# Kernel tuning notes

Measured on AMD Instinct MI355X. Metric: run time of the kernel, lower is better.

## Reference

```python
import jax, jax.numpy as jnp
import numpy as np

HEAD_SIZE = 128
N_Q_HEADS = 32
N_KV_HEADS = 8
ROPE_THETA = 1000000.0
RMS_EPS = 1e-6


def rms_norm(x, w, eps=RMS_EPS):
    # normalize over last dim in fp32, like Qwen3RMSNorm
    xf = x.astype(jnp.float32)
    var = jnp.mean(xf * xf, axis=-1, keepdims=True)
    return w * (xf * jax.lax.rsqrt(var + eps)).astype(x.dtype)


def rope_cache(T, dim, theta=ROPE_THETA):
    half = dim // 2
    inv_freq = 1.0 / theta ** (jnp.arange(half, dtype=jnp.float32) / half)
    freqs = jnp.arange(T, dtype=jnp.float32)[:, None] * inv_freq[None, :]  # [T, half]
    emb = jnp.concatenate([freqs, freqs], axis=-1)  # [T, dim]
    return jnp.cos(emb), jnp.sin(emb)


def rotate_half(x):
    x1, x2 = jnp.split(x, 2, axis=-1)
    return jnp.concatenate([-x2, x1], axis=-1)


def setup_inputs() -> dict:
    key = jax.random.key(0)
    ks = jax.random.split(key, 5)
    B, T, C = 2, 2048, 4096
    s = 0.02
    return {
        "hidden_states": jax.random.normal(ks[0], (B, T, C), jnp.float32),
        "wq": jax.random.normal(ks[1], (N_Q_HEADS * HEAD_SIZE, C), jnp.float32) * s,
        "wk": jax.random.normal(ks[2], (N_KV_HEADS * HEAD_SIZE, C), jnp.float32) * s,
        "wv": jax.random.normal(ks[3], (N_KV_HEADS * HEAD_SIZE, C), jnp.float32) * s,
        "wo": jax.random.normal(ks[4], (C, N_Q_HEADS * HEAD_SIZE), jnp.float32) * s,
        "q_norm_w": jnp.ones((HEAD_SIZE,), jnp.float32),
        "k_norm_w": jnp.ones((HEAD_SIZE,), jnp.float32),
    }


def reference(hidden_states, wq, wk, wv, wo, q_norm_w, k_norm_w):
    B, T, C = hidden_states.shape
    D = HEAD_SIZE
    groups = N_Q_HEADS // N_KV_HEADS
    scale = D ** -0.5

    # projections -> [B, H, T, D]
    q = (hidden_states @ wq.T).reshape(B, T, N_Q_HEADS, D)
    k = (hidden_states @ wk.T).reshape(B, T, N_KV_HEADS, D)
    v = (hidden_states @ wv.T).reshape(B, T, N_KV_HEADS, D)

    q = rms_norm(q, q_norm_w).transpose(0, 2, 1, 3)
    k = rms_norm(k, k_norm_w).transpose(0, 2, 1, 3)
    v = v.transpose(0, 2, 1, 3)

    cos, sin = rope_cache(T, D)  # [T, D]
    cos = cos[None, None]  # broadcast over batch, heads
    sin = sin[None, None]
    q = q * cos + rotate_half(q) * sin
    k = k * cos + rotate_half(k) * sin

    # GQA repeat_kv: [B, Hkv, T, D] -> [B, Hq, T, D]
    k = jnp.repeat(k, groups, axis=1)
    v = jnp.repeat(v, groups, axis=1)

    # causal SDPA
    scores = jnp.einsum("bhqd,bhkd->bhqk", q, k) * scale
    causal = jnp.tril(jnp.ones((T, T), bool))
    scores = jnp.where(causal[None, None], scores, -jnp.inf)
    probs = jax.nn.softmax(scores, axis=-1)
    attn = jnp.einsum("bhqk,bhkd->bhqd", probs, v)

    attn = attn.transpose(0, 2, 1, 3).reshape(B, T, N_Q_HEADS * D)
    return attn @ wo.T
```

## Files before the change

### kernel.cpp

```cpp
#include <hip/hip_runtime.h>
#include <math.h>

typedef unsigned short u16;
typedef __attribute__((ext_vector_type(8))) short short8;
typedef __attribute__((ext_vector_type(4))) float f32x4;
typedef __attribute__((ext_vector_type(16))) float f32x16;

#define AS1 __attribute__((address_space(1)))
#define AS3 __attribute__((address_space(3)))

__device__ __forceinline__ void gload_lds16(const u16* g, u16* l) {
  __builtin_amdgcn_global_load_lds((AS1 void*)g, (AS3 void*)l, 16, 0, 0);
}

__device__ __forceinline__ float bf2f(u16 u) {
  union { unsigned i; float f; } c; c.i = ((unsigned)u) << 16; return c.f;
}
__device__ __forceinline__ u16 f2bf(float f) {
  union { float f; unsigned i; } c; c.f = f;
  unsigned r = c.i + 0x7fffu + ((c.i >> 16) & 1u);
  return (u16)(r >> 16);
}

__global__ __launch_bounds__(256)
void cvt_f32_bf16_k(const float* __restrict__ src, u16* __restrict__ dst, int n8)
{
  int i = blockIdx.x * blockDim.x + threadIdx.x;
  const int stride = gridDim.x * blockDim.x;
  for (; i < n8; i += stride) {
    float4 a = ((const float4*)src)[2 * i];
    float4 b = ((const float4*)src)[2 * i + 1];
    short8 o;
    o[0] = (short)f2bf(a.x); o[1] = (short)f2bf(a.y);
    o[2] = (short)f2bf(a.z); o[3] = (short)f2bf(a.w);
    o[4] = (short)f2bf(b.x); o[5] = (short)f2bf(b.y);
    o[6] = (short)f2bf(b.z); o[7] = (short)f2bf(b.w);
    ((short8*)dst)[i] = o;
  }
}

#define MFMA16(a, b, c) __builtin_amdgcn_mfma_f32_16x16x32_bf16((a), (b), (c), 0, 0, 0)

#define STAGE_H(panel, h, t, ldsb)                                          \
  { const u16* s_ = (panel) + (size_t)((h) * 128) * 4096 + (t) * 64;        \
    gload_lds16(s_,                   (ldsb) + ldst0);                      \
    gload_lds16(s_ + (size_t)64*4096, (ldsb) + 4096 + ldst0); }

#define PHASE(MB, STAGE_STMT, TAIL)                                         \
  {                                                                         \
    short8 a0k0 = *(const short8*)(aB + (MB)*1024 + aoff0);                 \
    short8 a0k1 = *(const short8*)(aB + (MB)*1024 + (aoff0 ^ 32));          \
    short8 a1k0 = *(const short8*)(aB + ((MB)+1)*1024 + aoff0);             \
    short8 a1k1 = *(const short8*)(aB + ((MB)+1)*1024 + (aoff0 ^ 32));      \
    STAGE_STMT                                                              \
    __builtin_amdgcn_s_barrier();                                           \
    asm volatile("s_waitcnt lgkmcnt(0)" ::: "memory");                      \
    __builtin_amdgcn_s_setprio(1);                                          \
    _Pragma("unroll")                                                       \
    for (int n = 0; n < 4; ++n) {                                           \
      acc[(MB)][n]   = MFMA16(a0k0, br[n][0], acc[(MB)][n]);                \
      acc[(MB)][n]   = MFMA16(a0k1, br[n][1], acc[(MB)][n]);                \
      acc[(MB)+1][n] = MFMA16(a1k0, br[n][0], acc[(MB)+1][n]);              \
      acc[(MB)+1][n] = MFMA16(a1k1, br[n][1], acc[(MB)+1][n]);              \
    }                                                                       \
    __builtin_amdgcn_s_setprio(0);                                          \
    TAIL                                                                    \
    __builtin_amdgcn_s_barrier();                                           \
  }

#define KTILE(BUF, T)                                                       \
  {                                                                         \
    const u16* aB = sA + (BUF) * 16384 + wr * 8192;                         \
    const u16* bB = sB + (BUF) * 16384 + (wc >> 1) * 8192;                  \
    u16* aO = sA + ((BUF) ^ 1) * 16384;                                     \
    u16* bO = sB + (BUF) * 16384;                                           \
    const bool st1 = (T) + 1 < NT, st2 = (T) + 2 < NT;                      \
    short8 br[4][2];                                                        \
    _Pragma("unroll")                                                       \
    for (int n = 0; n < 4; ++n) {                                           \
      br[n][0] = *(const short8*)(bB + n * 1024 + boff0);                   \
      br[n][1] = *(const short8*)(bB + n * 1024 + (boff0 ^ 32));            \
    }                                                                       \
    PHASE(0, if (st1) STAGE_H(aS, 0, (T) + 1, aO);, ;)                      \
    PHASE(2, if (st1) STAGE_H(aS, 1, (T) + 1, aO + 8192);, ;)               \
    PHASE(4, if (st2) STAGE_H(bS, 0, (T) + 2, bO);, ;)                      \
    PHASE(6, if (st2) STAGE_H(bS, 1, (T) + 2, bO + 8192);,                  \
          if ((T) < NT - 2) { asm volatile("s_waitcnt vmcnt(4)" ::: "memory"); } \
          else              { asm volatile("s_waitcnt vmcnt(0)" ::: "memory"); }) \
  }

template<int MODE, typename OutT>
__global__ __launch_bounds__(512, 2)
void gemm256(const u16* __restrict__ A, const u16* __restrict__ W0,
             const u16* __restrict__ W1, const u16* __restrict__ W2,
             OutT* __restrict__ C)
{
  constexpr int K = 4096;
  constexpr int NT = K / 64;
  constexpr int LDC = (MODE == 0) ? 6144 : 4096;
  constexpr int NBM = 16;
  constexpr int NBN = (MODE == 0) ? 24 : 16;
  constexpr int NWG = NBM * NBN;

  __shared__ __align__(16) u16 sA[2 * 16384];
  __shared__ __align__(16) u16 sB[2 * 16384];

  const int tid = threadIdx.x;
  const int wid = tid >> 6, lane = tid & 63;
  const int g = lane >> 4, li = lane & 15;
  const int wr = wid >> 2, wc = wid & 3;

  const int bid = blockIdx.x;
  const int wg = (bid & 7) * (NWG / 8) + (bid >> 3);
  const int bm = wg % NBM, bn = wg / NBM;
  const int n0 = bn * 256;

  const u16* Wp; int nrow0;
  if (MODE == 0) {
    if (n0 < 4096)      { Wp = W0; nrow0 = n0; }
    else if (n0 < 5120) { Wp = W1; nrow0 = n0 - 4096; }
    else                { Wp = W2; nrow0 = n0 - 5120; }
  } else { Wp = W0; nrow0 = n0; }

  const int r0 = tid >> 3;
  const int sc0 = (tid & 7) ^ (r0 & 7);
  const u16* aS = A  + (size_t)(bm * 256 + r0) * K + sc0 * 8;
  const u16* bS = Wp + (size_t)(nrow0   + r0) * K + sc0 * 8;
  const int ldst0 = wid * 512;

  const int aoff0 = li * 64 + ((g ^ (li & 7)) * 8);
  const int boff0 = (wc & 1) * 4096 + aoff0;

  f32x4 acc[8][4] = {};

  STAGE_H(bS, 0, 0, sB);
  STAGE_H(bS, 1, 0, sB + 8192);
  STAGE_H(aS, 0, 0, sA);
  STAGE_H(aS, 1, 0, sA + 8192);
  STAGE_H(bS, 0, 1, sB + 16384);
  STAGE_H(bS, 1, 1, sB + 24576);
  asm volatile("s_waitcnt vmcnt(4)" ::: "memory");
  __builtin_amdgcn_s_barrier();

  for (int t = 0; t < NT; t += 2) {
    KTILE(0, t)
    KTILE(1, t + 1)
  }

#pragma unroll
  for (int m = 0; m < 8; ++m)
#pragma unroll
    for (int n = 0; n < 4; ++n)
#pragma unroll
      for (int j = 0; j < 4; ++j) {
        int row = bm * 256 + wr * 128 + m * 16 + g * 4 + j;
        int col = n0 + wc * 64 + n * 16 + li;
        float v = acc[m][n][j];
        if constexpr (sizeof(OutT) == 2) C[(size_t)row * LDC + col] = (OutT)f2bf(v);
        else                             C[(size_t)row * LDC + col] = (OutT)v;
      }
}

__global__ __launch_bounds__(256)
void norm_rope(const u16* __restrict__ qkv, const float* __restrict__ qw,
               const float* __restrict__ kw, u16* __restrict__ Qo,
               u16* __restrict__ Ko)
{
  const int tid = threadIdx.x;
  const int wid = tid >> 6, l = tid & 63;
  const int idx = blockIdx.x * 4 + wid;

  const u16* src; const float* w; u16* dst; int t;
  if (idx < 131072) {
    int row = idx >> 5, h = idx & 31;
    int b = row >> 11; t = row & 2047;
    src = qkv + (size_t)row * 6144 + h * 128;
    w = qw;
    dst = Qo + (((size_t)(b * 32 + h)) * 2048 + t) * 128;
  } else {
    int j = idx - 131072;
    int row = j >> 3, hk = j & 7;
    int b = row >> 11; t = row & 2047;
    src = qkv + (size_t)row * 6144 + 4096 + hk * 128;
    w = kw;
    dst = Ko + (((size_t)(b * 8 + hk)) * 2048 + t) * 128;
  }

  float x1 = bf2f(src[l]), x2 = bf2f(src[l + 64]);
  float ss = x1 * x1 + x2 * x2;
#pragma unroll
  for (int off = 32; off; off >>= 1) ss += __shfl_xor(ss, off);
  float rn = rsqrtf(ss * (1.0f / 128.0f) + 1e-6f);
  float y1 = x1 * rn * w[l];
  float y2 = x2 * rn * w[l + 64];

  float ang = (float)t * expf((float)l * -0.21586735246819178f);
  float c = cosf(ang), s = sinf(ang);
  dst[l]      = f2bf(y1 * c - y2 * s);
  dst[l + 64] = f2bf(y2 * c + y1 * s);
}

__global__ __launch_bounds__(256)
void transpose_v(const u16* __restrict__ qkv, u16* __restrict__ Vt)
{
  const int tblk = blockIdx.x, bh = blockIdx.y;
  const int b = bh >> 3, hk = bh & 7;
  const int tid = threadIdx.x;
  __shared__ __align__(16) u16 tile[64][136];

#pragma unroll
  for (int r = 0; r < 4; ++r) {
    int u = tid + r * 256;
    int row = u >> 4, cu = u & 15;
    short8 v = *(const short8*)(qkv + (size_t)(b * 2048 + tblk * 64 + row) * 6144
                                + 5120 + hk * 128 + cu * 8);
    *(short8*)(&tile[row][cu * 8]) = v;
  }
  __syncthreads();
#pragma unroll
  for (int it = 0; it < 4; ++it) {
    int u = tid + it * 256;
    int d = u & 127, tg = u >> 7;
    short8 wv8;
#pragma unroll
    for (int j = 0; j < 8; ++j) wv8[j] = (short)tile[tg * 8 + j][d];
    *(short8*)(Vt + ((size_t)(b * 8 + hk) * 128 + d) * 2048 + tblk * 64 + tg * 8) = wv8;
  }
}

__global__ __launch_bounds__(256, 2)
void attn_fwd(const u16* __restrict__ Q, const u16* __restrict__ Kc,
              const u16* __restrict__ Vt, u16* __restrict__ O)
{
  const int qt = 15 - (int)blockIdx.x;
  const int bh = blockIdx.y;
  const int b = bh >> 5, h = bh & 31, hkv = h >> 2;
  const int tid = threadIdx.x, wid = tid >> 6;
  const int lane = tid & 63, ql = lane & 31, hi = lane >> 5;

  __shared__ __align__(16) u16 sK[2][64 * 128];
  __shared__ __align__(16) u16 sV[2][128 * 64];

  const u16* Kb = Kc + ((size_t)(b * 8 + hkv)) * 2048 * 128;
  const u16* Vb = Vt + ((size_t)(b * 8 + hkv)) * 128 * 2048;

  const int kr0 = tid >> 4;
  const u16* kSrc = Kb + (size_t)kr0 * 128 + (((tid & 15) ^ (kr0 & 7)) * 8);
  const int vr0 = tid >> 3;
  const u16* vSrc = Vb + (size_t)vr0 * 2048 + (((tid & 7) ^ (vr0 & 7)) * 8);
  u16* const kDst = (u16*)sK[0] + wid * 512;
  u16* const vDst = (u16*)sV[0] + wid * 512;

  const int qg = qt * 128 + wid * 32 + ql;
  const u16* qrow = Q + ((size_t)(b * 32 + h) * 2048 + qg) * 128;
  short8 qf[8];
#pragma unroll
  for (int m = 0; m < 8; ++m) qf[m] = *(const short8*)(qrow + m * 16 + hi * 8);

  f32x16 oacc[4] = {};
  float mrun = -INFINITY, lrun = 0.f;
  const float scale = 0.08838834764831845f;
  const int nt = 2 * qt + 2;

#pragma unroll
  for (int p = 0; p < 4; ++p) {
    gload_lds16(kSrc + p * 2048,  kDst + p * 2048);
    gload_lds16(vSrc + p * 65536, vDst + p * 2048);
  }
  asm volatile("s_waitcnt vmcnt(0)" ::: "memory");
  __builtin_amdgcn_s_barrier();

  int cur = 0;
  for (int kt = 0; kt < nt; ++kt) {
    const int kv0 = kt * 64;
    if (kt + 1 < nt) {
      const u16* ks = kSrc + (size_t)(kv0 + 64) * 128;
      const u16* vs = vSrc + (kv0 + 64);
      u16* kd = kDst + (cur ^ 1) * 8192;
      u16* vd = vDst + (cur ^ 1) * 8192;
#pragma unroll
      for (int p = 0; p < 4; ++p) {
        gload_lds16(ks + p * 2048,  kd + p * 2048);
        gload_lds16(vs + p * 65536, vd + p * 2048);
      }
    }
    const u16* sKc = sK[cur];
    const u16* sVc = sV[cur];

    f32x16 P0 = {}, P1 = {};
    __builtin_amdgcn_s_setprio(1);
#pragma unroll
    for (int m = 0; m < 8; ++m) {
      const int c0 = ((m * 2 + hi) ^ (ql & 7)) * 8;
      short8 k0 = *(const short8*)(sKc + ql * 128 + c0);
      short8 k1 = *(const short8*)(sKc + (32 + ql) * 128 + c0);
      P0 = __builtin_amdgcn_mfma_f32_32x32x16_bf16(k0, qf[m], P0, 0, 0, 0);
      P1 = __builtin_amdgcn_mfma_f32_32x32x16_bf16(k1, qf[m], P1, 0, 0, 0);
    }
    __builtin_amdgcn_s_setprio(0);

#pragma unroll
    for (int r = 0; r < 16; ++r) {
      const int kvl = (r & 3) + 8 * (r >> 2) + 4 * hi;
      float v0 = P0[r] * scale; if (kv0 + kvl > qg)      v0 = -INFINITY; P0[r] = v0;
      float v1 = P1[r] * scale; if (kv0 + 32 + kvl > qg) v1 = -INFINITY; P1[r] = v1;
    }

    float pmax = -INFINITY;
#pragma unroll
    for (int r = 0; r < 16; ++r) pmax = fmaxf(pmax, fmaxf(P0[r], P1[r]));
    pmax = fmaxf(pmax, __shfl_xor(pmax, 32));

    if (!__all(pmax - mrun <= 8.f)) {
      float mnew = fmaxf(mrun, pmax);
      float corr = __expf(mrun - mnew);
      lrun *= corr;
      mrun = mnew;
#pragma unroll
      for (int r = 0; r < 16; ++r) {
        int qidx = (r & 3) + 8 * (r >> 2) + 4 * hi;
        float cr = __shfl(corr, qidx);
#pragma unroll
        for (int dt = 0; dt < 4; ++dt) oacc[dt][r] *= cr;
      }
    }

    float psum = 0.f;
#pragma unroll
    for (int r = 0; r < 16; ++r) {
      float e0 = __expf(P0[r] - mrun); P0[r] = e0; psum += e0;
      float e1 = __expf(P1[r] - mrun); P1[r] = e1; psum += e1;
    }
    psum += __shfl_xor(psum, 32);
    lrun += psum;

    __builtin_amdgcn_s_setprio(1);
#pragma unroll
    for (int s = 0; s < 4; ++s) {
      const int R0 = 8 * (s & 1), R1 = R0 + 4;
      float a0 = (s < 2) ? P0[R0 + 0] : P1[R0 + 0];
      float a1 = (s < 2) ? P0[R0 + 1] : P1[R0 + 1];
      float a2 = (s < 2) ? P0[R0 + 2] : P1[R0 + 2];
      float a3 = (s < 2) ? P0[R0 + 3] : P1[R0 + 3];
      float b0 = (s < 2) ? P0[R1 + 0] : P1[R1 + 0];
      float b1 = (s < 2) ? P0[R1 + 1] : P1[R1 + 1];
      float b2 = (s < 2) ? P0[R1 + 2] : P1[R1 + 2];
      float b3 = (s < 2) ? P0[R1 + 3] : P1[R1 + 3];
      unsigned y0, y1, z0, z1;
      asm("v_cvt_pk_bf16_f32 %0, %1, %2" : "=v"(y0) : "v"(a0), "v"(a1));
      asm("v_cvt_pk_bf16_f32 %0, %1, %2" : "=v"(z0) : "v"(b0), "v"(b1));
      asm("v_cvt_pk_bf16_f32 %0, %1, %2" : "=v"(y1) : "v"(a2), "v"(a3));
      asm("v_cvt_pk_bf16_f32 %0, %1, %2" : "=v"(z1) : "v"(b2), "v"(b3));
      asm("v_permlane32_swap_b32 %0, %1" : "+v"(y0), "+v"(z0));
      asm("v_permlane32_swap_b32 %0, %1" : "+v"(y1), "+v"(z1));
      union { unsigned u[4]; short8 v; } pa;
      pa.u[0] = y0; pa.u[1] = y1; pa.u[2] = z0; pa.u[3] = z1;
#pragma unroll
      for (int dt = 0; dt < 4; ++dt) {
        const int c = ((s * 2 + hi) ^ (ql & 7)) * 8;
        short8 vf = *(const short8*)(sVc + (dt * 32 + ql) * 64 + c);
        oacc[dt] = __builtin_amdgcn_mfma_f32_32x32x16_bf16(pa.v, vf, oacc[dt], 0, 0, 0);
      }
    }
    __builtin_amdgcn_s_setprio(0);

    asm volatile("s_waitcnt lgkmcnt(0)" ::: "memory");
    asm volatile("s_waitcnt vmcnt(0)" ::: "memory");
    __builtin_amdgcn_s_barrier();
    cur ^= 1;
  }

  float inv = 1.f / lrun;
  const int qbase = b * 2048 + qt * 128 + wid * 32;
#pragma unroll
  for (int r = 0; r < 16; ++r) {
    const int qidx = (r & 3) + 8 * (r >> 2) + 4 * hi;
    float ir = __shfl(inv, qidx);
    size_t base = (size_t)(qbase + qidx) * 4096 + h * 128 + ql;
#pragma unroll
    for (int dt = 0; dt < 4; ++dt)
      O[base + dt * 32] = f2bf(oacc[dt][r] * ir);
  }
}

extern "C" void kernel_launch(void* const* d_in, const int* in_sizes, int n_in,
                              void* d_out, int out_size, void* d_ws, size_t ws_size,
                              hipStream_t stream) {
  const float* hs  = (const float*)d_in[0];
  const float* wq  = (const float*)d_in[1];
  const float* wk  = (const float*)d_in[2];
  const float* wv  = (const float*)d_in[3];
  const float* wo  = (const float*)d_in[4];
  const float* qnw = (const float*)d_in[5];
  const float* knw = (const float*)d_in[6];
  float* out = (float*)d_out;

  char* ws = (char*)d_ws;
  u16* qkv = (u16*)(ws);
  u16* qr  = (u16*)(ws + 50331648);
  u16* kr  = (u16*)(ws + 83886080);
  u16* vt  = (u16*)(ws + 92274688);
  u16* hsb = (u16*)(ws + 100663296);
  u16* wqb = (u16*)(ws + 134217728);
  u16* wkb = (u16*)(ws + 167772160);
  u16* wvb = (u16*)(ws + 176160768);
  u16* ao  = (u16*)(ws);
  u16* wob = qr;

  cvt_f32_bf16_k<<<dim3(2048), dim3(256), 0, stream>>>(hs, hsb, 16777216 / 8);
  cvt_f32_bf16_k<<<dim3(2048), dim3(256), 0, stream>>>(wq, wqb, 16777216 / 8);
  cvt_f32_bf16_k<<<dim3(1024), dim3(256), 0, stream>>>(wk, wkb, 4194304 / 8);
  cvt_f32_bf16_k<<<dim3(1024), dim3(256), 0, stream>>>(wv, wvb, 4194304 / 8);

  gemm256<0, u16><<<dim3(384), dim3(512), 0, stream>>>(hsb, wqb, wkb, wvb, qkv);
  norm_rope<<<dim3(40960), dim3(256), 0, stream>>>(qkv, qnw, knw, qr, kr);
  transpose_v<<<dim3(32, 16), dim3(256), 0, stream>>>(qkv, vt);
  attn_fwd<<<dim3(16, 64), dim3(256), 0, stream>>>(qr, kr, vt, ao);

  cvt_f32_bf16_k<<<dim3(2048), dim3(256), 0, stream>>>(wo, wob, 16777216 / 8);
  gemm256<1, float><<<dim3(256), dim3(512), 0, stream>>>(ao, wob, nullptr, nullptr, out);
}
```

Before: 610.7 us.

## Merge input conversions into one launch and move global-to-LDS staging after MFMA

```diff
diff --git a/kernel.cpp b/kernel.cpp
--- a/kernel.cpp
+++ b/kernel.cpp
@@ -39,6 +39,31 @@
   }
 }
 
+__global__ __launch_bounds__(256)
+void cvt_batch4(const float* __restrict__ s0, u16* __restrict__ d0,
+                const float* __restrict__ s1, u16* __restrict__ d1,
+                const float* __restrict__ s2, u16* __restrict__ d2,
+                const float* __restrict__ s3, u16* __restrict__ d3)
+{
+  int i = blockIdx.x * blockDim.x + threadIdx.x;
+  const int stride = gridDim.x * blockDim.x;
+  for (; i < 5242880; i += stride) {
+    const float* s; u16* d; int j;
+    if (i < 2097152)      { s = s0; d = d0; j = i; }
+    else if (i < 4194304) { s = s1; d = d1; j = i - 2097152; }
+    else if (i < 4718592) { s = s2; d = d2; j = i - 4194304; }
+    else                  { s = s3; d = d3; j = i - 4718592; }
+    float4 a = ((const float4*)s)[2 * j];
+    float4 b = ((const float4*)s)[2 * j + 1];
+    short8 o;
+    o[0] = (short)f2bf(a.x); o[1] = (short)f2bf(a.y);
+    o[2] = (short)f2bf(a.z); o[3] = (short)f2bf(a.w);
+    o[4] = (short)f2bf(b.x); o[5] = (short)f2bf(b.y);
+    o[6] = (short)f2bf(b.z); o[7] = (short)f2bf(b.w);
+    ((short8*)d)[j] = o;
+  }
+}
+
 #define MFMA16(a, b, c) __builtin_amdgcn_mfma_f32_16x16x32_bf16((a), (b), (c), 0, 0, 0)
 
 #define STAGE_H(panel, h, t, ldsb)                                          \
@@ -52,7 +77,6 @@
     short8 a0k1 = *(const short8*)(aB + (MB)*1024 + (aoff0 ^ 32));          \
     short8 a1k0 = *(const short8*)(aB + ((MB)+1)*1024 + aoff0);             \
     short8 a1k1 = *(const short8*)(aB + ((MB)+1)*1024 + (aoff0 ^ 32));      \
-    STAGE_STMT                                                              \
     __builtin_amdgcn_s_barrier();                                           \
     asm volatile("s_waitcnt lgkmcnt(0)" ::: "memory");                      \
     __builtin_amdgcn_s_setprio(1);                                          \
@@ -64,8 +88,8 @@
       acc[(MB)+1][n] = MFMA16(a1k1, br[n][1], acc[(MB)+1][n]);              \
     }                                                                       \
     __builtin_amdgcn_s_setprio(0);                                          \
+    STAGE_STMT                                                              \
     TAIL                                                                    \
-    __builtin_amdgcn_s_barrier();                                           \
   }
 
 #define KTILE(BUF, T)                                                       \
@@ -86,7 +110,8 @@
     PHASE(4, if (st2) STAGE_H(bS, 0, (T) + 2, bO);, ;)                      \
     PHASE(6, if (st2) STAGE_H(bS, 1, (T) + 2, bO + 8192);,                  \
           if ((T) < NT - 2) { asm volatile("s_waitcnt vmcnt(4)" ::: "memory"); } \
-          else              { asm volatile("s_waitcnt vmcnt(0)" ::: "memory"); }) \
+          else              { asm volatile("s_waitcnt vmcnt(0)" ::: "memory"); } \
+          __builtin_amdgcn_s_barrier();)                                    \
   }
 
 template<int MODE, typename OutT>
@@ -405,18 +430,15 @@
   u16* wkb = (u16*)(ws + 167772160);
   u16* wvb = (u16*)(ws + 176160768);
   u16* ao  = (u16*)(ws);
-  u16* wob = qr;
-
-  cvt_f32_bf16_k<<<dim3(2048), dim3(256), 0, stream>>>(hs, hsb, 16777216 / 8);
-  cvt_f32_bf16_k<<<dim3(2048), dim3(256), 0, stream>>>(wq, wqb, 16777216 / 8);
-  cvt_f32_bf16_k<<<dim3(1024), dim3(256), 0, stream>>>(wk, wkb, 4194304 / 8);
-  cvt_f32_bf16_k<<<dim3(1024), dim3(256), 0, stream>>>(wv, wvb, 4194304 / 8);
+  u16* wob = hsb;
+
+  cvt_batch4<<<dim3(2048), dim3(256), 0, stream>>>(hs, hsb, wq, wqb, wk, wkb, wv, wvb);
 
   gemm256<0, u16><<<dim3(384), dim3(512), 0, stream>>>(hsb, wqb, wkb, wvb, qkv);
+  cvt_f32_bf16_k<<<dim3(2048), dim3(256), 0, stream>>>(wo, wob, 16777216 / 8);
   norm_rope<<<dim3(40960), dim3(256), 0, stream>>>(qkv, qnw, knw, qr, kr);
   transpose_v<<<dim3(32, 16), dim3(256), 0, stream>>>(qkv, vt);
   attn_fwd<<<dim3(16, 64), dim3(256), 0, stream>>>(qr, kr, vt, ao);
 
-  cvt_f32_bf16_k<<<dim3(2048), dim3(256), 0, stream>>>(wo, wob, 16777216 / 8);
   gemm256<1, float><<<dim3(256), dim3(512), 0, stream>>>(ao, wob, nullptr, nullptr, out);
 }
```

New measurement: 631.9 us. 1.03x slower.
